# Kernel tuning notes

Hardware: AMD Instinct MI355X
Metric: run time of the kernel (lower is better)

Reference implementation:

```python
import jax, jax.numpy as jnp
import numpy as np

B, L, D = 4, 4096, 1024


def setup_inputs() -> dict:
    key = jax.random.key(0)
    ks = jax.random.split(key, 10)
    x = jax.random.normal(ks[0], (B, L, D), dtype=jnp.float32)
    time_decay = jax.random.normal(ks[1], (D,), dtype=jnp.float32) * 0.1 - 5.0
    time_first = jax.random.normal(ks[2], (D,), dtype=jnp.float32) * 0.01
    time_mix_k = jnp.ones((D,), jnp.float32) * 0.5
    time_mix_v = jnp.ones((D,), jnp.float32) * 0.5
    time_mix_r = jnp.ones((D,), jnp.float32) * 0.5
    s = 1.0 / np.sqrt(D)
    Wk = jax.random.normal(ks[3], (D, D), dtype=jnp.float32) * s
    Wv = jax.random.normal(ks[4], (D, D), dtype=jnp.float32) * s
    Wr = jax.random.normal(ks[5], (D, D), dtype=jnp.float32) * s
    Wo = jax.random.normal(ks[6], (D, D), dtype=jnp.float32) * s
    return {"x": x, "time_decay": time_decay, "time_first": time_first,
            "time_mix_k": time_mix_k, "time_mix_v": time_mix_v, "time_mix_r": time_mix_r,
            "Wk": Wk, "Wv": Wv, "Wr": Wr, "Wo": Wo}


def _wkv_scan(k, v, w, u):
    # k, v: [B, L, D]; w, u: [D]. Sequential linear recurrence over L.
    decay = jnp.exp(w)  # per-channel decay factor e^{w}, w = -exp(time_decay) < 0
    Bb, Ll, Dd = k.shape

    def step(carry, kv_t):
        a, b = carry  # [B, D] numerator / denominator states
        k_t, v_t = kv_t
        ek_u = jnp.exp(u + k_t)
        wkv = (a + ek_u * v_t) / jnp.maximum(b + ek_u, 1e-6)
        ek = jnp.exp(k_t)
        return (decay * a + ek * v_t, decay * b + ek), wkv

    init = (jnp.zeros((Bb, Dd), k.dtype), jnp.zeros((Bb, Dd), k.dtype))
    _, out = jax.lax.scan(step, init, (jnp.swapaxes(k, 0, 1), jnp.swapaxes(v, 0, 1)))
    return jnp.swapaxes(out, 0, 1)  # [B, L, D]


def reference(x, time_decay, time_first, time_mix_k, time_mix_v, time_mix_r, Wk, Wv, Wr, Wo):
    Ll = x.shape[1]
    # token shift: x_prev[t] = x[t-1], zeros at t=0
    x_prev = jnp.pad(x, ((0, 0), (1, 0), (0, 0)))[:, :Ll]
    xk = x * time_mix_k + x_prev * (1.0 - time_mix_k)
    xv = x * time_mix_v + x_prev * (1.0 - time_mix_v)
    xr = x * time_mix_r + x_prev * (1.0 - time_mix_r)
    k = jnp.einsum('bld,ed->ble', xk, Wk)
    v = jnp.einsum('bld,ed->ble', xv, Wv)
    r = jax.nn.sigmoid(jnp.einsum('bld,ed->ble', xr, Wr))
    w = -jnp.exp(time_decay)
    wkv = _wkv_scan(k, v, w, time_first)
    return jnp.einsum('bld,ed->ble', r * wkv, Wo)
```

## Files before the change

### kernel.cpp

```cpp
#include <hip/hip_runtime.h>
#include <cstdint>
#include <cstddef>

typedef __bf16 bf16;
typedef __bf16 bf16x8 __attribute__((ext_vector_type(8)));
typedef float floatx4 __attribute__((ext_vector_type(4)));
typedef float floatx8 __attribute__((ext_vector_type(8)));
typedef unsigned int u32;

constexpr int Bb = 4, Ll = 4096, Dd = 1024;
constexpr int M  = Bb * Ll;
constexpr int NC = 64, CT = 64;

typedef const __attribute__((address_space(1))) u32 glb_u32;
typedef __attribute__((address_space(3))) u32 lds_u32;
__device__ __forceinline__ void gld16(const bf16* g, bf16* l) {
  __builtin_amdgcn_global_load_lds((glb_u32*)g, (lds_u32*)l, 16, 0, 0);
}
__device__ __forceinline__ void bar() {
  __builtin_amdgcn_s_barrier();
  asm volatile("" ::: "memory");
}

__global__ __launch_bounds__(256) void convw(
    const float* __restrict__ W, bf16* __restrict__ Wb)
{
  size_t base = ((size_t)blockIdx.x * 256 + threadIdx.x) * 8;
  floatx8 w = *(const floatx8*)(W + base);
  bf16x8 o;
  #pragma unroll
  for (int j = 0; j < 8; ++j) o[j] = (bf16)w[j];
  *(bf16x8*)(Wb + base) = o;
}

__global__ __launch_bounds__(256) void convw3(
    const float* __restrict__ Wa, const float* __restrict__ Wbp, const float* __restrict__ Wc,
    bf16* __restrict__ oa, bf16* __restrict__ ob, bf16* __restrict__ oc)
{
  const float* s = blockIdx.y == 0 ? Wa : (blockIdx.y == 1 ? Wbp : Wc);
  bf16*        d = blockIdx.y == 0 ? oa : (blockIdx.y == 1 ? ob  : oc);
  size_t base = ((size_t)blockIdx.x * 256 + threadIdx.x) * 8;
  floatx8 w = *(const floatx8*)(s + base);
  bf16x8 o;
  #pragma unroll
  for (int j = 0; j < 8; ++j) o[j] = (bf16)w[j];
  *(bf16x8*)(d + base) = o;
}

__global__ __launch_bounds__(256) void prep3(
    const float* __restrict__ x, const float* __restrict__ ma, const float* __restrict__ mb,
    const float* __restrict__ mc,
    bf16* __restrict__ oa, bf16* __restrict__ ob, bf16* __restrict__ oc)
{
  size_t base = ((size_t)blockIdx.x * 256 + threadIdx.x) * 8;
  int d = (int)(base & (size_t)(Dd - 1));
  int l = (int)((base / Dd) & (size_t)(Ll - 1));
  floatx8 xc = *(const floatx8*)(x + base);
  floatx8 xp = l ? *(const floatx8*)(x + base - Dd) : (floatx8)(0.0f);
  floatx8 a = *(const floatx8*)(ma + d);
  floatx8 b = *(const floatx8*)(mb + d);
  floatx8 c = *(const floatx8*)(mc + d);
  bf16x8 ra, rb, rc;
  #pragma unroll
  for (int j = 0; j < 8; ++j) {
    ra[j] = (bf16)(xc[j] * a[j] + xp[j] * (1.0f - a[j]));
    rb[j] = (bf16)(xc[j] * b[j] + xp[j] * (1.0f - b[j]));
    rc[j] = (bf16)(xc[j] * c[j] + xp[j] * (1.0f - c[j]));
  }
  *(bf16x8*)(oa + base) = ra;
  *(bf16x8*)(ob + base) = rb;
  *(bf16x8*)(oc + base) = rc;
}

template <int ACT>
__global__ __launch_bounds__(512, 2) void gemm8(
    const bf16* __restrict__ A, const bf16* __restrict__ W, void* __restrict__ Cout)
{
  __shared__ __align__(16) bf16 sm[65536];
  const int tid  = threadIdx.x;
  const int lane = tid & 63;
  const int w    = tid >> 6;
  const int wm   = (w >> 2) * 128;
  const int wn   = (w & 3) * 64;
  const int fr   = lane & 15;
  const int cu   = lane >> 4;
  const int key  = fr & 7;
  const int sw0  = ((cu)     ^ key) * 8;
  const int sw1  = ((4 | cu) ^ key) * 8;
  const int aro  = wm + fr;
  const int bro  = wn + fr;

  const int flat = (int)(blockIdx.y * 4 + blockIdx.x);
  const int nid  = (flat & 7) * 32 + (flat >> 3);
  const int m0   = (nid >> 2) * 256, n0 = (nid & 3) * 256;

  const int w0_ = tid, w1_ = tid + 512;
  const int lr0 = w0_ >> 3, sc0 = ((w0_ & 7) ^ (lr0 & 7)) * 8;
  const int lr1 = w1_ >> 3, sc1 = ((w1_ & 7) ^ (lr1 & 7)) * 8;
  const size_t rA0 = (size_t)(m0 + lr0) * Dd + sc0;
  const size_t rA1 = (size_t)(m0 + lr1) * Dd + sc1;
  const size_t rB0 = (size_t)(n0 + lr0) * Dd + sc0;
  const size_t rB1 = (size_t)(n0 + lr1) * Dd + sc1;
  const size_t HSTEP = (size_t)128 * Dd;

  floatx4 acc[8][4];
  #pragma unroll
  for (int i = 0; i < 8; ++i)
    #pragma unroll
    for (int j = 0; j < 4; ++j)
      acc[i][j] = (floatx4)(0.0f);

  {
    bf16* A0 = sm;
    bf16* B0 = sm + 16384;
    gld16(A + rA0,         A0 + (size_t)w0_ * 8);
    gld16(A + rA1,         A0 + (size_t)w1_ * 8);
    gld16(W + rB0,         B0 + (size_t)w0_ * 8);
    gld16(W + rB1,         B0 + (size_t)w1_ * 8);
    gld16(W + rB0 + HSTEP, B0 + 8192 + (size_t)w0_ * 8);
    gld16(W + rB1 + HSTEP, B0 + 8192 + (size_t)w1_ * 8);
    gld16(A + rA0 + HSTEP, A0 + 8192 + (size_t)w0_ * 8);
    gld16(A + rA1 + HSTEP, A0 + 8192 + (size_t)w1_ * 8);
    asm volatile("s_waitcnt vmcnt(4)" ::: "memory");
    bar();
  }

  bf16x8 a[8], bl[4], bh[4];
  #pragma unroll 2
  for (int t = 0; t < 16; ++t) {
    const int p = t & 1;
    bf16* Ap = sm + p * 32768;
    bf16* Bp = Ap + 16384;
    bf16* Aq = sm + (p ^ 1) * 32768;
    bf16* Bq = Aq + 16384;
    const size_t kn = (size_t)((t < 15 ? t + 1 : 15) * 64);

    #pragma unroll
    for (int i = 0; i < 4; ++i) {
      a[i * 2 + 0] = *(const bf16x8*)(Ap + (aro + i * 16) * 64 + sw0);
      a[i * 2 + 1] = *(const bf16x8*)(Ap + (aro + i * 16) * 64 + sw1);
    }
    #pragma unroll
    for (int j = 0; j < 2; ++j) {
      bl[j * 2 + 0] = *(const bf16x8*)(Bp + (bro + j * 16) * 64 + sw0);
      bl[j * 2 + 1] = *(const bf16x8*)(Bp + (bro + j * 16) * 64 + sw1);
    }
    gld16(A + rA0 + kn, Aq + (size_t)w0_ * 8);
    gld16(A + rA1 + kn, Aq + (size_t)w1_ * 8);
    asm volatile("s_waitcnt lgkmcnt(8)" ::: "memory");
    bar();
    __builtin_amdgcn_s_setprio(1);
    #pragma unroll
    for (int ks = 0; ks < 2; ++ks)
      #pragma unroll
      for (int i = 0; i < 4; ++i)
        #pragma unroll
        for (int j = 0; j < 2; ++j)
          acc[i][j] = __builtin_amdgcn_mfma_f32_16x16x32_bf16(a[i * 2 + ks], bl[j * 2 + ks], acc[i][j], 0, 0, 0);
    __builtin_amdgcn_s_setprio(0);
    bar();

    #pragma unroll
    for (int j = 0; j < 2; ++j) {
      bh[j * 2 + 0] = *(const bf16x8*)(Bp + (bro + (j + 2) * 16) * 64 + sw0);
      bh[j * 2 + 1] = *(const bf16x8*)(Bp + (bro + (j + 2) * 16) * 64 + sw1);
    }
    gld16(W + rB0 + kn, Bq + (size_t)w0_ * 8);
    gld16(W + rB1 + kn, Bq + (size_t)w1_ * 8);
    asm volatile("s_waitcnt vmcnt(4)" ::: "memory");
    bar();
    __builtin_amdgcn_s_setprio(1);
    #pragma unroll
    for (int ks = 0; ks < 2; ++ks)
      #pragma unroll
      for (int i = 0; i < 4; ++i)
        #pragma unroll
        for (int j = 0; j < 2; ++j)
          acc[i][j + 2] = __builtin_amdgcn_mfma_f32_16x16x32_bf16(a[i * 2 + ks], bh[j * 2 + ks], acc[i][j + 2], 0, 0, 0);
    __builtin_amdgcn_s_setprio(0);
    bar();

    #pragma unroll
    for (int i = 0; i < 4; ++i) {
      a[i * 2 + 0] = *(const bf16x8*)(Ap + (aro + (i + 4) * 16) * 64 + sw0);
      a[i * 2 + 1] = *(const bf16x8*)(Ap + (aro + (i + 4) * 16) * 64 + sw1);
    }
    gld16(W + rB0 + kn + HSTEP, Bq + 8192 + (size_t)w0_ * 8);
    gld16(W + rB1 + kn + HSTEP, Bq + 8192 + (size_t)w1_ * 8);
    bar();
    __builtin_amdgcn_s_setprio(1);
    #pragma unroll
    for (int ks = 0; ks < 2; ++ks)
      #pragma unroll
      for (int i = 0; i < 4; ++i)
        #pragma unroll
        for (int j = 0; j < 2; ++j)
          acc[i + 4][j + 2] = __builtin_amdgcn_mfma_f32_16x16x32_bf16(a[i * 2 + ks], bh[j * 2 + ks], acc[i + 4][j + 2], 0, 0, 0);
    __builtin_amdgcn_s_setprio(0);
    bar();

    gld16(A + rA0 + kn + HSTEP, Aq + 8192 + (size_t)w0_ * 8);
    gld16(A + rA1 + kn + HSTEP, Aq + 8192 + (size_t)w1_ * 8);
    asm volatile("s_waitcnt vmcnt(4)" ::: "memory");
    bar();
    __builtin_amdgcn_s_setprio(1);
    #pragma unroll
    for (int ks = 0; ks < 2; ++ks)
      #pragma unroll
      for (int i = 0; i < 4; ++i)
        #pragma unroll
        for (int j = 0; j < 2; ++j)
          acc[i + 4][j] = __builtin_amdgcn_mfma_f32_16x16x32_bf16(a[i * 2 + ks], bl[j * 2 + ks], acc[i + 4][j], 0, 0, 0);
    __builtin_amdgcn_s_setprio(0);
    bar();
  }
  asm volatile("s_waitcnt vmcnt(0)" ::: "memory");

  #pragma unroll
  for (int mi = 0; mi < 8; ++mi) {
    int rbase = m0 + wm + mi * 16 + (lane >> 4) * 4;
    #pragma unroll
    for (int j = 0; j < 4; ++j) {
      int col = n0 + wn + j * 16 + (lane & 15);
      #pragma unroll
      for (int r = 0; r < 4; ++r) {
        float v = acc[mi][j][r];
        size_t off = (size_t)(rbase + r) * Dd + col;
        if (ACT == 0)      ((float*)Cout)[off] = v;
        else if (ACT == 1) ((bf16*)Cout)[off]  = (bf16)(1.0f / (1.0f + __expf(-v)));
        else               ((bf16*)Cout)[off]  = (bf16)v;
      }
    }
  }
}

__global__ __launch_bounds__(256) void scan_partial(
    const bf16* __restrict__ k, const bf16* __restrict__ v,
    const float* __restrict__ td, float* __restrict__ Pa, float* __restrict__ Pb)
{
  int d = blockIdx.x * 256 + threadIdx.x;
  int b = blockIdx.y, c = blockIdx.z;
  float decay = __expf(-__expf(td[d]));
  size_t base = ((size_t)(b * Ll + c * CT)) * Dd + d;
  float pa = 0.0f, pb = 0.0f;
  #pragma unroll 4
  for (int t = 0; t < CT; ++t) {
    size_t idx = base + (size_t)t * Dd;
    float ek = __expf((float)k[idx]);
    pa = decay * pa + ek * (float)v[idx];
    pb = decay * pb + ek;
  }
  size_t o = ((size_t)(b * NC + c)) * Dd + d;
  Pa[o] = pa; Pb[o] = pb;
}

__global__ __launch_bounds__(256) void scan_combine(
    const float* __restrict__ td, const float* __restrict__ Pa, const float* __restrict__ Pb,
    float* __restrict__ A0, float* __restrict__ B0)
{
  int d = blockIdx.x * 256 + threadIdx.x;
  int b = blockIdx.y;
  float dT = __expf(-__expf(td[d]) * (float)CT);
  float a = 0.0f, bb = 0.0f;
  for (int c = 0; c < NC; ++c) {
    size_t o = ((size_t)(b * NC + c)) * Dd + d;
    A0[o] = a; B0[o] = bb;
    a  = dT * a  + Pa[o];
    bb = dT * bb + Pb[o];
  }
}

__global__ __launch_bounds__(256) void scan_final(
    const bf16* __restrict__ k, bf16* __restrict__ vy, const bf16* __restrict__ r,
    const float* __restrict__ td, const float* __restrict__ tf,
    const float* __restrict__ A0, const float* __restrict__ B0)
{
  int d = blockIdx.x * 256 + threadIdx.x;
  int b = blockIdx.y, c = blockIdx.z;
  float decay = __expf(-__expf(td[d]));
  float u     = tf[d];
  size_t o = ((size_t)(b * NC + c)) * Dd + d;
  float a = A0[o], bb = B0[o];
  size_t base = ((size_t)(b * Ll + c * CT)) * Dd + d;
  for (int t = 0; t < CT; ++t) {
    size_t idx = base + (size_t)t * Dd;
    float kk = (float)k[idx];
    float vv = (float)vy[idx];
    float eku = __expf(u + kk);
    float wkv = (a + eku * vv) / fmaxf(bb + eku, 1e-6f);
    vy[idx] = (bf16)((float)r[idx] * wkv);
    float ek = __expf(kk);
    a  = decay * a  + ek * vv;
    bb = decay * bb + ek;
  }
}

extern "C" void kernel_launch(void* const* d_in, const int* in_sizes, int n_in,
                              void* d_out, int out_size, void* d_ws, size_t ws_size,
                              hipStream_t stream)
{
  const float* x  = (const float*)d_in[0];
  const float* td = (const float*)d_in[1];
  const float* tf = (const float*)d_in[2];
  const float* mk = (const float*)d_in[3];
  const float* mv = (const float*)d_in[4];
  const float* mr = (const float*)d_in[5];
  const float* Wk = (const float*)d_in[6];
  const float* Wv = (const float*)d_in[7];
  const float* Wr = (const float*)d_in[8];
  const float* Wo = (const float*)d_in[9];
  float* out = (float*)d_out;

  char* ws = (char*)d_ws;
  const size_t S2 = (size_t)M * Dd * sizeof(bf16);
  const size_t SP = (size_t)Bb * NC * Dd;
  bf16* buf1 = (bf16*)(ws);
  bf16* buf2 = (bf16*)(ws + S2);
  bf16* buf3 = (bf16*)(ws + 2 * S2);
  float* Pa = (float*)(ws + 3 * S2);
  float* Pb = Pa + SP;
  float* A0 = Pb + SP;
  float* B0 = A0 + SP;

  char* ob  = (char*)d_out;
  bf16* rr  = (bf16*)d_out;
  bf16* Wkb = (bf16*)(ob + ((size_t)32 << 20));
  bf16* Wvb = (bf16*)(ob + ((size_t)34 << 20));
  bf16* Wrb = (bf16*)(ob + ((size_t)36 << 20));
  bf16* Wob = (bf16*)Pa;

  dim3 gp((unsigned)((size_t)M * Dd / (256 * 8)));
  dim3 gw((unsigned)((size_t)Dd * Dd / (256 * 8)));
  dim3 gg(Dd / 256, M / 256);

  convw3<<<dim3(gw.x, 3), 256, 0, stream>>>(Wk, Wv, Wr, Wkb, Wvb, Wrb);

  prep3<<<gp, 256, 0, stream>>>(x, mk, mv, mr, buf1, buf2, buf3);

  gemm8<1><<<gg, 512, 0, stream>>>(buf3, Wrb, rr);
  gemm8<2><<<gg, 512, 0, stream>>>(buf1, Wkb, buf3);
  gemm8<2><<<gg, 512, 0, stream>>>(buf2, Wvb, buf1);

  scan_partial<<<dim3(Dd / 256, Bb, NC), 256, 0, stream>>>(buf3, buf1, td, Pa, Pb);
  scan_combine<<<dim3(Dd / 256, Bb), 256, 0, stream>>>(td, Pa, Pb, A0, B0);
  convw<<<gw, 256, 0, stream>>>(Wo, Wob);
  scan_final  <<<dim3(Dd / 256, Bb, NC), 256, 0, stream>>>(buf3, buf1, rr, td, tf, A0, B0);

  gemm8<0><<<gg, 512, 0, stream>>>(buf1, Wob, out);
}
```

Baseline: 338.3 us.

## Vectorize scan kernels to 4 channels per thread and regroup GEMM prefetches

The scan_partial and scan_final kernels now handle four adjacent channels per thread with 8-byte bf16x4 loads and stores, and a single block covers all 1024 channels of one (batch, chunk) pair. The intent is to cut the number of load instructions and improve memory coalescing in these bandwidth-bound passes, at the cost of four times fewer threads and therefore less parallelism to hide latency. The GEMM main loop is also restructured: both halves of the next A tile are issued together, then both halves of B, followed by one vmcnt(0) wait, replacing the staggered partial waits and the lgkmcnt wait. This changes how global-to-LDS loads overlap with the MFMA phases, and a full drain of outstanding loads can stall the pipeline.

```diff
diff --git a/kernel.cpp b/kernel.cpp
--- a/kernel.cpp
+++ b/kernel.cpp
@@ -3,6 +3,7 @@
 #include <cstddef>
 
 typedef __bf16 bf16;
+typedef __bf16 bf16x4 __attribute__((ext_vector_type(4)));
 typedef __bf16 bf16x8 __attribute__((ext_vector_type(8)));
 typedef float floatx4 __attribute__((ext_vector_type(4)));
 typedef float floatx8 __attribute__((ext_vector_type(8)));
@@ -115,13 +116,13 @@
     bf16* B0 = sm + 16384;
     gld16(A + rA0,         A0 + (size_t)w0_ * 8);
     gld16(A + rA1,         A0 + (size_t)w1_ * 8);
+    gld16(A + rA0 + HSTEP, A0 + 8192 + (size_t)w0_ * 8);
+    gld16(A + rA1 + HSTEP, A0 + 8192 + (size_t)w1_ * 8);
     gld16(W + rB0,         B0 + (size_t)w0_ * 8);
     gld16(W + rB1,         B0 + (size_t)w1_ * 8);
     gld16(W + rB0 + HSTEP, B0 + 8192 + (size_t)w0_ * 8);
     gld16(W + rB1 + HSTEP, B0 + 8192 + (size_t)w1_ * 8);
-    gld16(A + rA0 + HSTEP, A0 + 8192 + (size_t)w0_ * 8);
-    gld16(A + rA1 + HSTEP, A0 + 8192 + (size_t)w1_ * 8);
-    asm volatile("s_waitcnt vmcnt(4)" ::: "memory");
+    asm volatile("s_waitcnt vmcnt(0)" ::: "memory");
     bar();
   }
 
@@ -145,9 +146,10 @@
       bl[j * 2 + 0] = *(const bf16x8*)(Bp + (bro + j * 16) * 64 + sw0);
       bl[j * 2 + 1] = *(const bf16x8*)(Bp + (bro + j * 16) * 64 + sw1);
     }
-    gld16(A + rA0 + kn, Aq + (size_t)w0_ * 8);
-    gld16(A + rA1 + kn, Aq + (size_t)w1_ * 8);
-    asm volatile("s_waitcnt lgkmcnt(8)" ::: "memory");
+    gld16(A + rA0 + kn,         Aq + (size_t)w0_ * 8);
+    gld16(A + rA1 + kn,         Aq + (size_t)w1_ * 8);
+    gld16(A + rA0 + kn + HSTEP, Aq + 8192 + (size_t)w0_ * 8);
+    gld16(A + rA1 + kn + HSTEP, Aq + 8192 + (size_t)w1_ * 8);
     bar();
     __builtin_amdgcn_s_setprio(1);
     #pragma unroll
@@ -165,9 +167,10 @@
       bh[j * 2 + 0] = *(const bf16x8*)(Bp + (bro + (j + 2) * 16) * 64 + sw0);
       bh[j * 2 + 1] = *(const bf16x8*)(Bp + (bro + (j + 2) * 16) * 64 + sw1);
     }
-    gld16(W + rB0 + kn, Bq + (size_t)w0_ * 8);
-    gld16(W + rB1 + kn, Bq + (size_t)w1_ * 8);
-    asm volatile("s_waitcnt vmcnt(4)" ::: "memory");
+    gld16(W + rB0 + kn,         Bq + (size_t)w0_ * 8);
+    gld16(W + rB1 + kn,         Bq + (size_t)w1_ * 8);
+    gld16(W + rB0 + kn + HSTEP, Bq + 8192 + (size_t)w0_ * 8);
+    gld16(W + rB1 + kn + HSTEP, Bq + 8192 + (size_t)w1_ * 8);
     bar();
     __builtin_amdgcn_s_setprio(1);
     #pragma unroll
@@ -185,8 +188,6 @@
       a[i * 2 + 0] = *(const bf16x8*)(Ap + (aro + (i + 4) * 16) * 64 + sw0);
       a[i * 2 + 1] = *(const bf16x8*)(Ap + (aro + (i + 4) * 16) * 64 + sw1);
     }
-    gld16(W + rB0 + kn + HSTEP, Bq + 8192 + (size_t)w0_ * 8);
-    gld16(W + rB1 + kn + HSTEP, Bq + 8192 + (size_t)w1_ * 8);
     bar();
     __builtin_amdgcn_s_setprio(1);
     #pragma unroll
@@ -199,9 +200,7 @@
     __builtin_amdgcn_s_setprio(0);
     bar();
 
-    gld16(A + rA0 + kn + HSTEP, Aq + 8192 + (size_t)w0_ * 8);
-    gld16(A + rA1 + kn + HSTEP, Aq + 8192 + (size_t)w1_ * 8);
-    asm volatile("s_waitcnt vmcnt(4)" ::: "memory");
+    asm volatile("s_waitcnt vmcnt(0)" ::: "memory");
     bar();
     __builtin_amdgcn_s_setprio(1);
     #pragma unroll
@@ -238,20 +237,35 @@
     const bf16* __restrict__ k, const bf16* __restrict__ v,
     const float* __restrict__ td, float* __restrict__ Pa, float* __restrict__ Pb)
 {
-  int d = blockIdx.x * 256 + threadIdx.x;
-  int b = blockIdx.y, c = blockIdx.z;
-  float decay = __expf(-__expf(td[d]));
-  size_t base = ((size_t)(b * Ll + c * CT)) * Dd + d;
-  float pa = 0.0f, pb = 0.0f;
+  const int pair = blockIdx.x;
+  const int b = pair >> 6, c = pair & (NC - 1);
+  const int d0 = threadIdx.x * 4;
+  floatx4 tdv = *(const floatx4*)(td + d0);
+  float decay[4], pa[4], pb[4];
+  #pragma unroll
+  for (int j = 0; j < 4; ++j) {
+    decay[j] = __expf(-__expf(tdv[j]));
+    pa[j] = 0.0f; pb[j] = 0.0f;
+  }
+  size_t base = ((size_t)(b * Ll + c * CT)) * Dd + d0;
   #pragma unroll 4
   for (int t = 0; t < CT; ++t) {
     size_t idx = base + (size_t)t * Dd;
-    float ek = __expf((float)k[idx]);
-    pa = decay * pa + ek * (float)v[idx];
-    pb = decay * pb + ek;
-  }
-  size_t o = ((size_t)(b * NC + c)) * Dd + d;
-  Pa[o] = pa; Pb[o] = pb;
+    bf16x4 kk = *(const bf16x4*)(k + idx);
+    bf16x4 vv = *(const bf16x4*)(v + idx);
+    #pragma unroll
+    for (int j = 0; j < 4; ++j) {
+      float ek = __expf((float)kk[j]);
+      pa[j] = decay[j] * pa[j] + ek * (float)vv[j];
+      pb[j] = decay[j] * pb[j] + ek;
+    }
+  }
+  size_t o = (size_t)pair * Dd + d0;
+  floatx4 outa, outb;
+  #pragma unroll
+  for (int j = 0; j < 4; ++j) { outa[j] = pa[j]; outb[j] = pb[j]; }
+  *(floatx4*)(Pa + o) = outa;
+  *(floatx4*)(Pb + o) = outb;
 }
 
 __global__ __launch_bounds__(256) void scan_combine(
@@ -275,23 +289,40 @@
     const float* __restrict__ td, const float* __restrict__ tf,
     const float* __restrict__ A0, const float* __restrict__ B0)
 {
-  int d = blockIdx.x * 256 + threadIdx.x;
-  int b = blockIdx.y, c = blockIdx.z;
-  float decay = __expf(-__expf(td[d]));
-  float u     = tf[d];
-  size_t o = ((size_t)(b * NC + c)) * Dd + d;
-  float a = A0[o], bb = B0[o];
-  size_t base = ((size_t)(b * Ll + c * CT)) * Dd + d;
+  const int pair = blockIdx.x;
+  const int b = pair >> 6, c = pair & (NC - 1);
+  const int d0 = threadIdx.x * 4;
+  floatx4 tdv = *(const floatx4*)(td + d0);
+  floatx4 tfv = *(const floatx4*)(tf + d0);
+  size_t o = (size_t)pair * Dd + d0;
+  floatx4 av = *(const floatx4*)(A0 + o);
+  floatx4 bv = *(const floatx4*)(B0 + o);
+  float decay[4], u[4], a[4], bb[4];
+  #pragma unroll
+  for (int j = 0; j < 4; ++j) {
+    decay[j] = __expf(-__expf(tdv[j]));
+    u[j] = tfv[j]; a[j] = av[j]; bb[j] = bv[j];
+  }
+  size_t base = ((size_t)(b * Ll + c * CT)) * Dd + d0;
+  #pragma unroll 2
   for (int t = 0; t < CT; ++t) {
     size_t idx = base + (size_t)t * Dd;
-    float kk = (float)k[idx];
-    float vv = (float)vy[idx];
-    float eku = __expf(u + kk);
-    float wkv = (a + eku * vv) / fmaxf(bb + eku, 1e-6f);
-    vy[idx] = (bf16)((float)r[idx] * wkv);
-    float ek = __expf(kk);
-    a  = decay * a  + ek * vv;
-    bb = decay * bb + ek;
+    bf16x4 kk = *(const bf16x4*)(k + idx);
+    bf16x4 vv = *(const bf16x4*)(vy + idx);
+    bf16x4 rr4 = *(const bf16x4*)(r + idx);
+    bf16x4 y;
+    #pragma unroll
+    for (int j = 0; j < 4; ++j) {
+      float kkj = (float)kk[j];
+      float vvj = (float)vv[j];
+      float eku = __expf(u[j] + kkj);
+      float wkv = (a[j] + eku * vvj) / fmaxf(bb[j] + eku, 1e-6f);
+      y[j] = (bf16)((float)rr4[j] * wkv);
+      float ek = __expf(kkj);
+      a[j]  = decay[j] * a[j]  + ek * vvj;
+      bb[j] = decay[j] * bb[j] + ek;
+    }
+    *(bf16x4*)(vy + idx) = y;
   }
 }
 
@@ -341,10 +372,10 @@
   gemm8<2><<<gg, 512, 0, stream>>>(buf1, Wkb, buf3);
   gemm8<2><<<gg, 512, 0, stream>>>(buf2, Wvb, buf1);
 
-  scan_partial<<<dim3(Dd / 256, Bb, NC), 256, 0, stream>>>(buf3, buf1, td, Pa, Pb);
+  scan_partial<<<dim3(Bb * NC), 256, 0, stream>>>(buf3, buf1, td, Pa, Pb);
   scan_combine<<<dim3(Dd / 256, Bb), 256, 0, stream>>>(td, Pa, Pb, A0, B0);
   convw<<<gw, 256, 0, stream>>>(Wo, Wob);
-  scan_final  <<<dim3(Dd / 256, Bb, NC), 256, 0, stream>>>(buf3, buf1, rr, td, tf, A0, B0);
+  scan_final  <<<dim3(Bb * NC), 256, 0, stream>>>(buf3, buf1, rr, td, tf, A0, B0);
 
   gemm8<0><<<gg, 512, 0, stream>>>(buf1, Wob, out);
 }
```

Result: no change. 338.3 us (-0.0%).
